# Kernel optimization log

Hardware: AMD Instinct MI355X
Metric: run time of the kernel (lower is better)

Reference implementation:

```python
import jax, jax.numpy as jnp
import numpy as np

B, T, IN = 4096, 64, 3
D, H, NB = 128, 4, 2
DH = D // H  # 32
EPS = 1e-5


def layer_norm(x, g, b):
    mu = x.mean(-1, keepdims=True)
    v = x.var(-1, keepdims=True)
    return (x - mu) / jnp.sqrt(v + EPS) * g + b


def group_norm(x, g, b):
    # headwise GroupNorm over the last dim split into H groups of DH
    xr = x.reshape(x.shape[:-1] + (H, DH))
    mu = xr.mean(-1, keepdims=True)
    v = xr.var(-1, keepdims=True)
    xn = ((xr - mu) / jnp.sqrt(v + EPS)).reshape(x.shape)
    return xn * g + b


def slstm(xg, R):
    # xg: [B,T,4,D] input-driven gate preactivations (i,f,z,o)
    # R : [4,H,DH,DH] block-diagonal (per-head) recurrent kernels per gate
    Bb = xg.shape[0]

    def step(carry, g):
        h, c, n, m = carry  # each [B,D]
        r = jnp.einsum('bhd,ghde->bghe', h.reshape(Bb, H, DH), R).reshape(Bb, 4, D)
        g = g + r
        it, ft, zt, ot = g[:, 0], g[:, 1], g[:, 2], g[:, 3]
        m_new = jnp.maximum(ft + m, it)          # stabilizer state
        i = jnp.exp(it - m_new)                  # stabilized exp input gate
        f = jnp.exp(ft + m - m_new)              # stabilized exp forget gate
        c_new = f * c + i * jnp.tanh(zt)
        n_new = f * n + i                        # normalizer state
        h_new = jax.nn.sigmoid(ot) * c_new / n_new
        return (h_new, c_new, n_new, m_new), h_new

    init = tuple(jnp.zeros((Bb, D), xg.dtype) for _ in range(4))
    _, hs = jax.lax.scan(step, init, jnp.swapaxes(xg, 0, 1))  # [T,B,D]
    return jnp.swapaxes(hs, 0, 1)


def setup_inputs() -> dict:
    key = jax.random.key(0)
    ks = jax.random.split(key, 12)
    s_in = 1.0 / np.sqrt(IN)
    s_d = 1.0 / np.sqrt(D)
    inp = {
        'x': jax.random.normal(ks[0], (B, T, IN), jnp.float32),
        'w_in': jax.random.normal(ks[1], (IN, D), jnp.float32) * s_in,
        'b_in': jnp.zeros((D,), jnp.float32),
        'ln1_g': jnp.ones((NB, D), jnp.float32),
        'ln1_b': jnp.zeros((NB, D), jnp.float32),
        'Wg': jax.random.normal(ks[2], (NB, D, 4 * D), jnp.float32) * s_d,
        'bg': jnp.zeros((NB, 4 * D), jnp.float32),
        'Rg': jax.random.normal(ks[3], (NB, 4, H, DH, DH), jnp.float32) / np.sqrt(DH),
        'gn_g': jnp.ones((NB, D), jnp.float32),
        'gn_b': jnp.zeros((NB, D), jnp.float32),
        'ln2_g': jnp.ones((NB, D), jnp.float32),
        'ln2_b': jnp.zeros((NB, D), jnp.float32),
        'W1': jax.random.normal(ks[4], (NB, D, D), jnp.float32) * s_d,
        'W2': jax.random.normal(ks[5], (NB, D, D), jnp.float32) * s_d,
        'lnf_g': jnp.ones((D,), jnp.float32),
        'lnf_b': jnp.zeros((D,), jnp.float32),
        'w_out': jax.random.normal(ks[6], (D, 1), jnp.float32) * s_d,
        'b_out': jnp.zeros((1,), jnp.float32),
    }
    return inp


def reference(x, w_in, b_in, ln1_g, ln1_b, Wg, bg, Rg, gn_g, gn_b,
              ln2_g, ln2_b, W1, W2, lnf_g, lnf_b, w_out, b_out):
    h = x @ w_in + b_in  # [B,T,D]
    for blk in range(NB):
        # sLSTM sub-block (pre-LN residual)
        xn = layer_norm(h, ln1_g[blk], ln1_b[blk])
        xg = (xn @ Wg[blk] + bg[blk]).reshape(h.shape[0], T, 4, D)
        hs = slstm(xg, Rg[blk])
        h = h + group_norm(hs, gn_g[blk], gn_b[blk])
        # FFN sub-block (pre-LN residual, proj_factor=1.0, gelu, no bias)
        yn = layer_norm(h, ln2_g[blk], ln2_b[blk])
        h = h + jax.nn.gelu(yn @ W1[blk]) @ W2[blk]
    h = layer_norm(h, lnf_g, lnf_b)  # post-blocks norm
    out = (h[:, -1, :] @ w_out + b_out)[:, 0]  # [B]
    return out
```

## Files before the change

kernel.cpp:

```cpp
#include <hip/hip_runtime.h>
#include <hip/hip_bf16.h>
#include <cstdint>
#include <cstddef>

#define EPS 1e-5f
#define BB 4096
#define TT 64
#define NBLK 2
#define MROWS (BB * TT)

typedef unsigned short ushort_t;
typedef __attribute__((ext_vector_type(8))) short short8;
typedef __attribute__((ext_vector_type(4))) float floatx4;

__device__ __forceinline__ ushort_t f2b(float f) {
    __hip_bfloat16 h = __float2bfloat16(f);
    return *reinterpret_cast<ushort_t*>(&h);
}
__device__ __forceinline__ float tanh_fast(float z) {
    return 1.f - 2.f / (__expf(2.f * z) + 1.f);
}
__device__ __forceinline__ float rcp_f(float x) {
    return __builtin_amdgcn_rcpf(x);
}
__device__ __forceinline__ void lds_barrier() {
    asm volatile("s_waitcnt lgkmcnt(0)\n\ts_barrier" ::: "memory");
}

template <int CTRL>
__device__ __forceinline__ float ror_add(float v) {
    int r = __builtin_amdgcn_update_dpp(
        0, __builtin_bit_cast(int, v), CTRL, 0xf, 0xf, false);
    return v + __builtin_bit_cast(float, r);
}
__device__ __forceinline__ float red16(float v) {
    v = ror_add<0x121>(v);
    v = ror_add<0x122>(v);
    v = ror_add<0x124>(v);
    v = ror_add<0x128>(v);
    return v;
}

__global__ __launch_bounds__(256) void k_cvtall(
    const float* __restrict__ Wg, const float* __restrict__ W1,
    const float* __restrict__ W2, ushort_t* __restrict__ Wgt,
    ushort_t* __restrict__ W1t, ushort_t* __restrict__ W2t) {
    int idx = blockIdx.x * 256 + threadIdx.x;
    if (idx < 2 * 512 * 128) {
        int blk = idx >> 16, r = idx & 65535;
        int k = r >> 9, n = r & 511;
        Wgt[(size_t)blk * 65536 + n * 128 + k] = f2b(Wg[idx]);
    } else if (idx < 2 * 512 * 128 + 2 * 128 * 128) {
        int i2 = idx - 2 * 512 * 128;
        int blk = i2 >> 14, r = i2 & 16383;
        int k = r >> 7, n = r & 127;
        W1t[(size_t)blk * 16384 + n * 128 + k] = f2b(W1[i2]);
    } else {
        int i2 = idx - (2 * 512 * 128 + 2 * 128 * 128);
        int blk = i2 >> 14, r = i2 & 16383;
        int k = r >> 7, n = r & 127;
        W2t[(size_t)blk * 16384 + n * 128 + k] = f2b(W2[i2]);
    }
}

template <bool EMBED, bool LASTONLY>
__global__ __launch_bounds__(512, 2) void k_gslstm(
    float* __restrict__ h, const float* __restrict__ x,
    const float* __restrict__ w_in, const float* __restrict__ b_in,
    const ushort_t* __restrict__ Wgt, const float* __restrict__ bg,
    const float* __restrict__ Rg,
    const float* __restrict__ ln1g, const float* __restrict__ ln1b,
    const float* __restrict__ gng, const float* __restrict__ gnb) {
    __shared__ float xg_ring[2][512][16];
    __shared__ ushort_t Afrag[2][16][136];
    __shared__ ushort_t tpose[4][16][40];

    const int tid = threadIdx.x;
    const int lane = tid & 63;
    const int wave = tid >> 6;
    const int q = lane >> 4;
    const int ml = lane & 15;
    const int b0 = blockIdx.x * 16;
    const int xc = ((q + (ml >> 1)) & 3) * 4;

    if (wave < 4) {
        const int p = wave;
        const int row = p * 4 + q;
        short8 WB[4][8];
#pragma unroll
        for (int ks = 0; ks < 4; ++ks)
#pragma unroll
            for (int s = 0; s < 8; ++s)
                WB[ks][s] = *(const short8*)(Wgt +
                    ((size_t)(p * 128 + s * 16 + ml) * 128 + ks * 32 + q * 8));
        float biasv[8];
#pragma unroll
        for (int s = 0; s < 8; ++s) biasv[s] = bg[p * 128 + s * 16 + ml];

        const float4 Lg0 = *(const float4*)(ln1g + ml * 8);
        const float4 Lg1 = *(const float4*)(ln1g + ml * 8 + 4);
        const float4 Lb0 = *(const float4*)(ln1b + ml * 8);
        const float4 Lb1 = *(const float4*)(ln1b + ml * 8 + 4);
        float4 W00{}, W01{}, W10{}, W11{}, W20{}, W21{}, BE0{}, BE1{};
        if (EMBED) {
            W00 = *(const float4*)(w_in + 0 * 128 + ml * 8);
            W01 = *(const float4*)(w_in + 0 * 128 + ml * 8 + 4);
            W10 = *(const float4*)(w_in + 1 * 128 + ml * 8);
            W11 = *(const float4*)(w_in + 1 * 128 + ml * 8 + 4);
            W20 = *(const float4*)(w_in + 2 * 128 + ml * 8);
            W21 = *(const float4*)(w_in + 2 * 128 + ml * 8 + 4);
            BE0 = *(const float4*)(b_in + ml * 8);
            BE1 = *(const float4*)(b_in + ml * 8 + 4);
        }

        auto issue_in = [&](int tt, float4& A, float4& B) {
            const float4* hp =
                (const float4*)(h + ((size_t)(b0 + row) * TT + tt) * 128 + ml * 8);
            A = hp[0]; B = hp[1];
        };
        auto issue_x = [&](int tt, float& x0, float& x1, float& x2) {
            const float* xp = x + ((size_t)(b0 + row) * TT + tt) * 3;
            x0 = xp[0]; x1 = xp[1]; x2 = xp[2];
        };
        auto embed_v = [&](float x0, float x1, float x2, float* v) {
            const float w0[8] = {W00.x, W00.y, W00.z, W00.w, W01.x, W01.y, W01.z, W01.w};
            const float w1[8] = {W10.x, W10.y, W10.z, W10.w, W11.x, W11.y, W11.z, W11.w};
            const float w2[8] = {W20.x, W20.y, W20.z, W20.w, W21.x, W21.y, W21.z, W21.w};
            const float be[8] = {BE0.x, BE0.y, BE0.z, BE0.w, BE1.x, BE1.y, BE1.z, BE1.w};
#pragma unroll
            for (int j = 0; j < 8; ++j)
                v[j] = x0 * w0[j] + x1 * w1[j] + x2 * w2[j] + be[j];
        };
        auto ln_stage = [&](const float* v, int aslot) {
            float s = 0.f, ss = 0.f;
#pragma unroll
            for (int j = 0; j < 8; ++j) { s += v[j]; ss += v[j] * v[j]; }
            s = red16(s);
            ss = red16(ss);
            float mu = s * (1.f / 128.f);
            float rstd = rsqrtf(ss * (1.f / 128.f) - mu * mu + EPS);
            const float gg[8] = {Lg0.x, Lg0.y, Lg0.z, Lg0.w, Lg1.x, Lg1.y, Lg1.z, Lg1.w};
            const float bbv[8] = {Lb0.x, Lb0.y, Lb0.z, Lb0.w, Lb1.x, Lb1.y, Lb1.z, Lb1.w};
            ushort_t pk[8];
#pragma unroll
            for (int j = 0; j < 8; ++j)
                pk[j] = f2b((v[j] - mu) * rstd * gg[j] + bbv[j]);
            *(short8*)&Afrag[aslot][row][ml * 8] = *(const short8*)pk;
        };
        auto gemm_stage = [&](int slot) {
            short8 af[4];
#pragma unroll
            for (int ks = 0; ks < 4; ++ks)
                af[ks] = *(const short8*)&Afrag[slot][ml][ks * 32 + q * 8];
            floatx4 acc[8];
#pragma unroll
            for (int s = 0; s < 8; ++s) {
                float b = biasv[s];
                acc[s] = (floatx4){b, b, b, b};
            }
#pragma unroll
            for (int ks = 0; ks < 4; ++ks)
#pragma unroll
                for (int s = 0; s < 8; ++s)
                    acc[s] = __builtin_amdgcn_mfma_f32_16x16x32_bf16(
                        af[ks], WB[ks][s], acc[s], 0, 0, 0);
#pragma unroll
            for (int s = 0; s < 8; ++s)
                *(floatx4*)&xg_ring[slot][p * 128 + s * 16 + ml][xc] = acc[s];
        };

        float4 pA0, pA1, pB0, pB1;
        float px0 = 0.f, px1 = 0.f, px2 = 0.f, qx0 = 0.f, qx1 = 0.f, qx2 = 0.f;
        {
            float v[8];
            if (EMBED) {
                float a0, a1, a2, d0, d1, d2v;
                issue_x(0, a0, a1, a2);
                issue_x(1, d0, d1, d2v);
                issue_x(2, px0, px1, px2);
                embed_v(a0, a1, a2, v);  ln_stage(v, 0);
                embed_v(d0, d1, d2v, v); ln_stage(v, 1);
            } else {
                float4 a0, a1, d0, d1;
                issue_in(0, a0, a1);
                issue_in(1, d0, d1);
                issue_in(2, pA0, pA1);
                *(float4*)v = a0; *(float4*)(v + 4) = a1; ln_stage(v, 0);
                *(float4*)v = d0; *(float4*)(v + 4) = d1; ln_stage(v, 1);
            }
        }
        lds_barrier();
        gemm_stage(0);
        lds_barrier();

#pragma unroll 1
        for (int t = 0; t < TT; t += 2) {
            if (t + 3 < TT) {
                if (EMBED) issue_x(t + 3, qx0, qx1, qx2);
                else       issue_in(t + 3, pB0, pB1);
            }
            gemm_stage((t + 1) & 1);
            if (t + 2 < TT) {
                float v[8];
                if (EMBED) embed_v(px0, px1, px2, v);
                else { *(float4*)v = pA0; *(float4*)(v + 4) = pA1; }
                ln_stage(v, t & 1);
            }
            lds_barrier();
            if (t + 4 < TT) {
                if (EMBED) issue_x(t + 4, px0, px1, px2);
                else       issue_in(t + 4, pA0, pA1);
            }
            if (t + 2 < TT) gemm_stage(t & 1);
            if (t + 3 < TT) {
                float v[8];
                if (EMBED) embed_v(qx0, qx1, qx2, v);
                else { *(float4*)v = pB0; *(float4*)(v + 4) = pB1; }
                ln_stage(v, (t + 1) & 1);
            }
            lds_barrier();
        }
    } else {
        __builtin_amdgcn_s_setprio(1);
        const int hd = wave - 4;
        short8 RB[4][2];
#pragma unroll
        for (int g = 0; g < 4; ++g)
#pragma unroll
            for (int d2 = 0; d2 < 2; ++d2) {
                ushort_t tmp[8];
#pragma unroll
                for (int j = 0; j < 8; ++j)
                    tmp[j] = f2b(Rg[(size_t)g * 4096 + hd * 1024 +
                                    (q * 8 + j) * 32 + d2 * 16 + ml]);
                RB[g][d2] = *(const short8*)tmp;
            }
        const float gng0 = gng[hd * 32 + ml], gng1 = gng[hd * 32 + 16 + ml];
        const float gnb0 = gnb[hd * 32 + ml], gnb1 = gnb[hd * 32 + 16 + ml];
        float we[3][2], beh[2];
        if (EMBED) {
#pragma unroll
            for (int d2 = 0; d2 < 2; ++d2) {
#pragma unroll
                for (int c = 0; c < 3; ++c)
                    we[c][d2] = w_in[c * 128 + hd * 32 + d2 * 16 + ml];
                beh[d2] = b_in[hd * 32 + d2 * 16 + ml];
            }
        }
        float cst[8], nst[8], mst[8];
#pragma unroll
        for (int i = 0; i < 8; ++i) { cst[i] = 0.f; nst[i] = 0.f; mst[i] = 0.f; }
        {
            ushort_t* tp = &tpose[hd][0][0];
            for (int i = lane; i < 16 * 40; i += 64) tp[i] = 0;
        }

        auto scan_iter = [&](int t) {
            const bool doGN = (!LASTONLY || t == TT - 1);
            float xv[4][3];
            float hg[4][2];
            if (doGN) {
                if (EMBED) {
#pragma unroll
                    for (int r = 0; r < 4; ++r) {
                        const float* xp =
                            x + ((size_t)(b0 + q * 4 + r) * TT + t) * 3;
                        xv[r][0] = xp[0]; xv[r][1] = xp[1]; xv[r][2] = xp[2];
                    }
                } else {
#pragma unroll
                    for (int r = 0; r < 4; ++r)
#pragma unroll
                        for (int d2 = 0; d2 < 2; ++d2)
                            hg[r][d2] = h[((size_t)(b0 + q * 4 + r) * TT + t) * 128 +
                                          hd * 32 + d2 * 16 + ml];
                }
            }
            short8 h8 = *(const short8*)&tpose[hd][ml][q * 8];
            floatx4 acc[4][2];
#pragma unroll
            for (int g = 0; g < 4; ++g)
#pragma unroll
                for (int d2 = 0; d2 < 2; ++d2)
                    acc[g][d2] = *(const floatx4*)
                        &xg_ring[t & 1][g * 128 + hd * 32 + d2 * 16 + ml][xc];
#pragma unroll
            for (int g = 0; g < 4; ++g)
#pragma unroll
                for (int d2 = 0; d2 < 2; ++d2)
                    acc[g][d2] = __builtin_amdgcn_mfma_f32_16x16x32_bf16(
                        h8, RB[g][d2], acc[g][d2], 0, 0, 0);
            float hv[2][4];
#pragma unroll
            for (int d2 = 0; d2 < 2; ++d2)
#pragma unroll
                for (int r = 0; r < 4; ++r) {
                    const int si = d2 * 4 + r;
                    float it = acc[0][d2][r], ft = acc[1][d2][r];
                    float zt = acc[2][d2][r], ot = acc[3][d2][r];
                    float mn = fmaxf(ft + mst[si], it);
                    float iv = __expf(it - mn);
                    float fv = __expf(ft + mst[si] - mn);
                    float e2 = __expf(2.f * zt);
                    float th = 1.f - 2.f * rcp_f(e2 + 1.f);
                    float cn = fv * cst[si] + iv * th;
                    float nn = fv * nst[si] + iv;
                    float eo = __expf(-ot);
                    hv[d2][r] = cn * rcp_f(nn + nn * eo);
                    cst[si] = cn; nst[si] = nn; mst[si] = mn;
                }
#pragma unroll
            for (int d2 = 0; d2 < 2; ++d2)
#pragma unroll
                for (int r = 0; r < 4; ++r)
                    tpose[hd][q * 4 + r][d2 * 16 + ml] = f2b(hv[d2][r]);
            if (doGN) {
                float hinv[4][2];
#pragma unroll
                for (int r = 0; r < 4; ++r)
#pragma unroll
                    for (int d2 = 0; d2 < 2; ++d2) {
                        if (EMBED)
                            hinv[r][d2] = xv[r][0] * we[0][d2] +
                                          xv[r][1] * we[1][d2] +
                                          xv[r][2] * we[2][d2] + beh[d2];
                        else
                            hinv[r][d2] = hg[r][d2];
                    }
                float s[4], ss[4];
#pragma unroll
                for (int r = 0; r < 4; ++r) {
                    s[r] = hv[0][r] + hv[1][r];
                    ss[r] = hv[0][r] * hv[0][r] + hv[1][r] * hv[1][r];
                }
#pragma unroll
                for (int r = 0; r < 4; ++r) {
                    s[r] = red16(s[r]);
                    ss[r] = red16(ss[r]);
                }
#pragma unroll
                for (int r = 0; r < 4; ++r) {
                    float mu = s[r] * (1.f / 32.f);
                    float rstd = rsqrtf(ss[r] * (1.f / 32.f) - mu * mu + EPS);
#pragma unroll
                    for (int d2 = 0; d2 < 2; ++d2) {
                        float gv = d2 ? gng1 : gng0;
                        float bv = d2 ? gnb1 : gnb0;
                        h[((size_t)(b0 + q * 4 + r) * TT + t) * 128 +
                          hd * 32 + d2 * 16 + ml] =
                            hinv[r][d2] + (hv[d2][r] - mu) * rstd * gv + bv;
                    }
                }
            }
        };

        lds_barrier();
        lds_barrier();
#pragma unroll 1
        for (int t = 0; t < TT; t += 2) {
            scan_iter(t);
            lds_barrier();
            scan_iter(t + 1);
            lds_barrier();
        }
    }
}

template <int NT>
__global__ __launch_bounds__(256, 3) void k_ffn_pipe(
    float* __restrict__ h, const ushort_t* __restrict__ W1t,
    const ushort_t* __restrict__ W2t,
    const float* __restrict__ lng, const float* __restrict__ lnb) {
    __shared__ float Hraw[32][132];
    __shared__ ushort_t T1[32][136];
    __shared__ __align__(16) char Ubuf[32 * 132 * 4];
    auto As = (ushort_t(*)[136])Ubuf;
    auto T2 = (float(*)[132])Ubuf;

    int tid = threadIdx.x;
    int lane = tid & 63, wave = tid >> 6;
    int q = lane >> 4, ml = lane & 15;
    int wn = wave * 32;
    int r = tid >> 3, qd = tid & 7;
    int hi = lane >> 5, lo = lane & 31;
    size_t base = (size_t)blockIdx.x * (32 * NT);

    short8 W1B[2][4];
#pragma unroll
    for (int jn = 0; jn < 2; ++jn)
#pragma unroll
        for (int ks = 0; ks < 4; ++ks)
            W1B[jn][ks] = *(const short8*)(W1t +
                ((size_t)(wn + jn * 16 + ml) * 128 + ks * 32 + q * 8));

    float4 cur[4], nxt[4];
#pragma unroll
    for (int k = 0; k < 4; ++k)
        cur[k] = *(const float4*)(h + (base + wave * 8 + 2 * k + hi) * 128 + lo * 4);

#pragma unroll 1
    for (int it = 0; it < NT; ++it) {
#pragma unroll
        for (int k = 0; k < 4; ++k)
            *(float4*)&Hraw[wave * 8 + 2 * k + hi][lo * 4] = cur[k];
        if (it + 1 < NT) {
#pragma unroll
            for (int k = 0; k < 4; ++k)
                nxt[k] = *(const float4*)(h +
                    (base + (it + 1) * 32 + wave * 8 + 2 * k + hi) * 128 + lo * 4);
        }
        lds_barrier();

        float4 hv[4];
#pragma unroll
        for (int k = 0; k < 4; ++k)
            hv[k] = *(const float4*)&Hraw[r][qd * 16 + k * 4];
        float s = 0.f, ss = 0.f;
#pragma unroll
        for (int k = 0; k < 4; ++k) {
            float4 v = hv[k];
            s += v.x + v.y + v.z + v.w;
            ss += v.x * v.x + v.y * v.y + v.z * v.z + v.w * v.w;
        }
        s += __shfl_xor(s, 1); ss += __shfl_xor(ss, 1);
        s += __shfl_xor(s, 2); ss += __shfl_xor(ss, 2);
        s += __shfl_xor(s, 4); ss += __shfl_xor(ss, 4);
        float mu = s * (1.f / 128.f);
        float rstd = rsqrtf(ss * (1.f / 128.f) - mu * mu + EPS);
#pragma unroll
        for (int kk = 0; kk < 2; ++kk) {
            float4 a = hv[2 * kk];
            float4 b = hv[2 * kk + 1];
            int c0 = qd * 16 + kk * 8;
            float4 g0 = *(const float4*)(lng + c0);
            float4 g1 = *(const float4*)(lng + c0 + 4);
            float4 b0 = *(const float4*)(lnb + c0);
            float4 b1 = *(const float4*)(lnb + c0 + 4);
            ushort_t p[8];
            p[0] = f2b((a.x - mu) * rstd * g0.x + b0.x);
            p[1] = f2b((a.y - mu) * rstd * g0.y + b0.y);
            p[2] = f2b((a.z - mu) * rstd * g0.z + b0.z);
            p[3] = f2b((a.w - mu) * rstd * g0.w + b0.w);
            p[4] = f2b((b.x - mu) * rstd * g1.x + b1.x);
            p[5] = f2b((b.y - mu) * rstd * g1.y + b1.y);
            p[6] = f2b((b.z - mu) * rstd * g1.z + b1.z);
            p[7] = f2b((b.w - mu) * rstd * g1.w + b1.w);
            *(short8*)&As[r][c0] = *(const short8*)p;
        }
        lds_barrier();

        floatx4 acc[2][2];
#pragma unroll
        for (int i = 0; i < 2; ++i)
#pragma unroll
            for (int j = 0; j < 2; ++j) acc[i][j] = (floatx4)0.f;
#pragma unroll
        for (int ks = 0; ks < 4; ++ks) {
            short8 af[2];
#pragma unroll
            for (int im = 0; im < 2; ++im)
                af[im] = *(const short8*)&As[im * 16 + ml][ks * 32 + q * 8];
#pragma unroll
            for (int im = 0; im < 2; ++im)
#pragma unroll
                for (int jn = 0; jn < 2; ++jn)
                    acc[im][jn] = __builtin_amdgcn_mfma_f32_16x16x32_bf16(
                        af[im], W1B[jn][ks], acc[im][jn], 0, 0, 0);
        }
#pragma unroll
        for (int im = 0; im < 2; ++im)
#pragma unroll
            for (int jn = 0; jn < 2; ++jn)
#pragma unroll
                for (int rr = 0; rr < 4; ++rr) {
                    float v = acc[im][jn][rr];
                    float u = 0.7978845608028654f * (v + 0.044715f * v * v * v);
                    float gv = 0.5f * v * (1.f + tanh_fast(u));
                    T1[im * 16 + q * 4 + rr][wn + jn * 16 + ml] = f2b(gv);
                }
        short8 W2B[2][4];
#pragma unroll
        for (int jn = 0; jn < 2; ++jn)
#pragma unroll
            for (int ks = 0; ks < 4; ++ks)
                W2B[jn][ks] = *(const short8*)(W2t +
                    ((size_t)(wn + jn * 16 + ml) * 128 + ks * 32 + q * 8));
        lds_barrier();

#pragma unroll
        for (int i = 0; i < 2; ++i)
#pragma unroll
            for (int j = 0; j < 2; ++j) acc[i][j] = (floatx4)0.f;
#pragma unroll
        for (int ks = 0; ks < 4; ++ks) {
            short8 af[2];
#pragma unroll
            for (int im = 0; im < 2; ++im)
                af[im] = *(const short8*)&T1[im * 16 + ml][ks * 32 + q * 8];
#pragma unroll
            for (int im = 0; im < 2; ++im)
#pragma unroll
                for (int jn = 0; jn < 2; ++jn)
                    acc[im][jn] = __builtin_amdgcn_mfma_f32_16x16x32_bf16(
                        af[im], W2B[jn][ks], acc[im][jn], 0, 0, 0);
        }
#pragma unroll
        for (int im = 0; im < 2; ++im)
#pragma unroll
            for (int jn = 0; jn < 2; ++jn)
#pragma unroll
                for (int rr = 0; rr < 4; ++rr)
                    T2[im * 16 + q * 4 + rr][wn + jn * 16 + ml] = acc[im][jn][rr];
        lds_barrier();

#pragma unroll
        for (int k = 0; k < 4; ++k) {
            float4 t2v = *(const float4*)&T2[wave * 8 + 2 * k + hi][lo * 4];
            float4 o;
            o.x = cur[k].x + t2v.x;
            o.y = cur[k].y + t2v.y;
            o.z = cur[k].z + t2v.z;
            o.w = cur[k].w + t2v.w;
            *(float4*)(h + (base + it * 32 + wave * 8 + 2 * k + hi) * 128 + lo * 4) = o;
        }
        if (it + 1 < NT) {
#pragma unroll
            for (int k = 0; k < 4; ++k) cur[k] = nxt[k];
        }
    }
}

__global__ __launch_bounds__(256, 6) void k_tail(
    const float* __restrict__ h, const ushort_t* __restrict__ W1t,
    const ushort_t* __restrict__ W2t,
    const float* __restrict__ lng, const float* __restrict__ lnb,
    const float* __restrict__ lnfg, const float* __restrict__ lnfb,
    const float* __restrict__ w_out, const float* __restrict__ b_out,
    float* __restrict__ out) {
    __shared__ __align__(16) char U[32 * 136 * 2 * 2];
    auto As = (ushort_t(*)[136])U;
    auto T1 = (ushort_t(*)[136])(U + 32 * 136 * 2);
    auto F = (float(*)[136])U;
    int tid = threadIdx.x;
    int lane = tid & 63, wave = tid >> 6;
    int q = lane >> 4, ml = lane & 15;
    int wn = wave * 32;
    size_t row0 = (size_t)blockIdx.x * 32;

    short8 W1B[2][4];
#pragma unroll
    for (int jn = 0; jn < 2; ++jn)
#pragma unroll
        for (int ks = 0; ks < 4; ++ks)
            W1B[jn][ks] = *(const short8*)(W1t +
                ((size_t)(wn + jn * 16 + ml) * 128 + ks * 32 + q * 8));

    int r = tid >> 3, qd = tid & 7;
    size_t grow = (row0 + r) * TT + (TT - 1);
    const float* hrow = h + grow * 128 + qd * 16;
    float s = 0.f, ss = 0.f;
#pragma unroll
    for (int k = 0; k < 4; ++k) {
        float4 v = ((const float4*)hrow)[k];
        s += v.x + v.y + v.z + v.w;
        ss += v.x * v.x + v.y * v.y + v.z * v.z + v.w * v.w;
    }
    s += __shfl_xor(s, 1); ss += __shfl_xor(ss, 1);
    s += __shfl_xor(s, 2); ss += __shfl_xor(ss, 2);
    s += __shfl_xor(s, 4); ss += __shfl_xor(ss, 4);
    float mu = s * (1.f / 128.f);
    float rstd = rsqrtf(ss * (1.f / 128.f) - mu * mu + EPS);
#pragma unroll
    for (int kk = 0; kk < 2; ++kk) {
        float4 a = ((const float4*)hrow)[2 * kk];
        float4 b = ((const float4*)hrow)[2 * kk + 1];
        int c0 = qd * 16 + kk * 8;
        float4 g0 = *(const float4*)(lng + c0);
        float4 g1 = *(const float4*)(lng + c0 + 4);
        float4 b0 = *(const float4*)(lnb + c0);
        float4 b1 = *(const float4*)(lnb + c0 + 4);
        ushort_t p[8];
        p[0] = f2b((a.x - mu) * rstd * g0.x + b0.x);
        p[1] = f2b((a.y - mu) * rstd * g0.y + b0.y);
        p[2] = f2b((a.z - mu) * rstd * g0.z + b0.z);
        p[3] = f2b((a.w - mu) * rstd * g0.w + b0.w);
        p[4] = f2b((b.x - mu) * rstd * g1.x + b1.x);
        p[5] = f2b((b.y - mu) * rstd * g1.y + b1.y);
        p[6] = f2b((b.z - mu) * rstd * g1.z + b1.z);
        p[7] = f2b((b.w - mu) * rstd * g1.w + b1.w);
        *(short8*)&As[r][c0] = *(const short8*)p;
    }
    lds_barrier();

    floatx4 acc[2][2];
#pragma unroll
    for (int i = 0; i < 2; ++i)
#pragma unroll
        for (int j = 0; j < 2; ++j) acc[i][j] = (floatx4)0.f;
#pragma unroll
    for (int ks = 0; ks < 4; ++ks) {
        short8 af[2];
#pragma unroll
        for (int im = 0; im < 2; ++im)
            af[im] = *(const short8*)&As[im * 16 + ml][ks * 32 + q * 8];
#pragma unroll
        for (int im = 0; im < 2; ++im)
#pragma unroll
            for (int jn = 0; jn < 2; ++jn)
                acc[im][jn] = __builtin_amdgcn_mfma_f32_16x16x32_bf16(
                    af[im], W1B[jn][ks], acc[im][jn], 0, 0, 0);
    }
#pragma unroll
    for (int im = 0; im < 2; ++im)
#pragma unroll
        for (int jn = 0; jn < 2; ++jn)
#pragma unroll
            for (int rr = 0; rr < 4; ++rr) {
                float v = acc[im][jn][rr];
                float u = 0.7978845608028654f * (v + 0.044715f * v * v * v);
                float gv = 0.5f * v * (1.f + tanh_fast(u));
                T1[im * 16 + q * 4 + rr][wn + jn * 16 + ml] = f2b(gv);
            }
    short8 W2B[2][4];
#pragma unroll
    for (int jn = 0; jn < 2; ++jn)
#pragma unroll
        for (int ks = 0; ks < 4; ++ks)
            W2B[jn][ks] = *(const short8*)(W2t +
                ((size_t)(wn + jn * 16 + ml) * 128 + ks * 32 + q * 8));
    lds_barrier();

    float rres[2][2][4];
#pragma unroll
    for (int im = 0; im < 2; ++im)
#pragma unroll
        for (int jn = 0; jn < 2; ++jn)
#pragma unroll
            for (int rr = 0; rr < 4; ++rr) {
                int rloc = im * 16 + q * 4 + rr;
                rres[im][jn][rr] = h[((row0 + rloc) * TT + (TT - 1)) * 128 +
                                     wn + jn * 16 + ml];
            }
#pragma unroll
    for (int i = 0; i < 2; ++i)
#pragma unroll
        for (int j = 0; j < 2; ++j) acc[i][j] = (floatx4)0.f;
#pragma unroll
    for (int ks = 0; ks < 4; ++ks) {
        short8 af[2];
#pragma unroll
        for (int im = 0; im < 2; ++im)
            af[im] = *(const short8*)&T1[im * 16 + ml][ks * 32 + q * 8];
#pragma unroll
        for (int im = 0; im < 2; ++im)
#pragma unroll
            for (int jn = 0; jn < 2; ++jn)
                acc[im][jn] = __builtin_amdgcn_mfma_f32_16x16x32_bf16(
                    af[im], W2B[jn][ks], acc[im][jn], 0, 0, 0);
    }
    lds_barrier();
#pragma unroll
    for (int im = 0; im < 2; ++im)
#pragma unroll
        for (int jn = 0; jn < 2; ++jn)
#pragma unroll
            for (int rr = 0; rr < 4; ++rr) {
                int rloc = im * 16 + q * 4 + rr;
                F[rloc][wn + jn * 16 + ml] = rres[im][jn][rr] + acc[im][jn][rr];
            }
    lds_barrier();

    float4 fv[4];
#pragma unroll
    for (int k = 0; k < 4; ++k)
        fv[k] = *(const float4*)&F[r][qd * 16 + k * 4];
    float s2 = 0.f, ss2 = 0.f;
#pragma unroll
    for (int k = 0; k < 4; ++k) {
        float4 v = fv[k];
        s2 += v.x + v.y + v.z + v.w;
        ss2 += v.x * v.x + v.y * v.y + v.z * v.z + v.w * v.w;
    }
    s2 += __shfl_xor(s2, 1); ss2 += __shfl_xor(ss2, 1);
    s2 += __shfl_xor(s2, 2); ss2 += __shfl_xor(ss2, 2);
    s2 += __shfl_xor(s2, 4); ss2 += __shfl_xor(ss2, 4);
    float mu2 = s2 * (1.f / 128.f);
    float rstd2 = rsqrtf(ss2 * (1.f / 128.f) - mu2 * mu2 + EPS);
    float dot = 0.f;
#pragma unroll
    for (int k = 0; k < 4; ++k) {
        int c0 = qd * 16 + k * 4;
        float4 g = *(const float4*)(lnfg + c0);
        float4 bb = *(const float4*)(lnfb + c0);
        float4 w = *(const float4*)(w_out + c0);
        dot += ((fv[k].x - mu2) * rstd2 * g.x + bb.x) * w.x +
               ((fv[k].y - mu2) * rstd2 * g.y + bb.y) * w.y +
               ((fv[k].z - mu2) * rstd2 * g.z + bb.z) * w.z +
               ((fv[k].w - mu2) * rstd2 * g.w + bb.w) * w.w;
    }
    dot += __shfl_xor(dot, 1);
    dot += __shfl_xor(dot, 2);
    dot += __shfl_xor(dot, 4);
    if (qd == 0) out[row0 + r] = dot + b_out[0];
}

extern "C" void kernel_launch(void* const* d_in, const int* in_sizes, int n_in,
                              void* d_out, int out_size, void* d_ws, size_t ws_size,
                              hipStream_t stream) {
    const float* x    = (const float*)d_in[0];
    const float* w_in = (const float*)d_in[1];
    const float* b_in = (const float*)d_in[2];
    const float* ln1g = (const float*)d_in[3];
    const float* ln1b = (const float*)d_in[4];
    const float* Wg   = (const float*)d_in[5];
    const float* bg   = (const float*)d_in[6];
    const float* Rg   = (const float*)d_in[7];
    const float* gng  = (const float*)d_in[8];
    const float* gnb  = (const float*)d_in[9];
    const float* ln2g = (const float*)d_in[10];
    const float* ln2b = (const float*)d_in[11];
    const float* W1   = (const float*)d_in[12];
    const float* W2   = (const float*)d_in[13];
    const float* lnfg = (const float*)d_in[14];
    const float* lnfb = (const float*)d_in[15];
    const float* wout = (const float*)d_in[16];
    const float* bout = (const float*)d_in[17];
    float* out = (float*)d_out;

    float* h = (float*)d_ws;
    ushort_t* Wgt = (ushort_t*)(h + (size_t)MROWS * 128);
    ushort_t* W1t = Wgt + 2 * 512 * 128;
    ushort_t* W2t = W1t + 2 * 128 * 128;

    k_cvtall<<<(2 * 512 * 128 + 4 * 128 * 128) / 256, 256, 0, stream>>>(
        Wg, W1, W2, Wgt, W1t, W2t);

    k_gslstm<true, false><<<BB / 16, 512, 0, stream>>>(
        h, x, w_in, b_in, Wgt, bg, Rg, ln1g, ln1b, gng, gnb);
    k_ffn_pipe<8><<<MROWS / 256, 256, 0, stream>>>(h, W1t, W2t, ln2g, ln2b);
    k_gslstm<false, true><<<BB / 16, 512, 0, stream>>>(
        h, nullptr, nullptr, nullptr, Wgt + (size_t)512 * 128, bg + 512,
        Rg + (size_t)16384, ln1g + 128, ln1b + 128, gng + 128, gnb + 128);
    k_tail<<<BB / 32, 256, 0, stream>>>(h, W1t + 16384, W2t + 16384,
                                        ln2g + 128, ln2b + 128,
                                        lnfg, lnfb, wout, bout, out);
}
```

Measured before the change: 330.0 us.

## Replace block-pipelined FFN kernel with barrier-free per-wave 16-row FFN

Rewrites the middle FFN kernel so that each wave independently handles 16 rows. It loads those rows straight into registers as MFMA A-fragments, computes LayerNorm with cross-lane shuffles, and runs both GEMMs using only private per-wave LDS scratch, so it needs no block barriers. This removes the block-wide s_barrier synchronisation and the staging of h through shared LDS. In exchange, every wave reloads all of W1 and W2 from global/L2, where before each block kept them in registers across 8 tiles. The grid also grows to many small blocks without the prefetch pipeline.

```diff
diff --git a/kernel.cpp b/kernel.cpp
--- a/kernel.cpp
+++ b/kernel.cpp
@@ -25,6 +25,9 @@
 }
 __device__ __forceinline__ void lds_barrier() {
     asm volatile("s_waitcnt lgkmcnt(0)\n\ts_barrier" ::: "memory");
+}
+__device__ __forceinline__ void ds_wait() {
+    asm volatile("s_waitcnt lgkmcnt(0)" ::: "memory");
 }
 
 template <int CTRL>
@@ -366,167 +369,110 @@
     }
 }
 
-template <int NT>
-__global__ __launch_bounds__(256, 3) void k_ffn_pipe(
+__global__ __launch_bounds__(256) void k_ffn_wave(
     float* __restrict__ h, const ushort_t* __restrict__ W1t,
     const ushort_t* __restrict__ W2t,
     const float* __restrict__ lng, const float* __restrict__ lnb) {
-    __shared__ float Hraw[32][132];
-    __shared__ ushort_t T1[32][136];
-    __shared__ __align__(16) char Ubuf[32 * 132 * 4];
-    auto As = (ushort_t(*)[136])Ubuf;
-    auto T2 = (float(*)[132])Ubuf;
-
-    int tid = threadIdx.x;
-    int lane = tid & 63, wave = tid >> 6;
-    int q = lane >> 4, ml = lane & 15;
-    int wn = wave * 32;
-    int r = tid >> 3, qd = tid & 7;
-    int hi = lane >> 5, lo = lane & 31;
-    size_t base = (size_t)blockIdx.x * (32 * NT);
-
-    short8 W1B[2][4];
-#pragma unroll
-    for (int jn = 0; jn < 2; ++jn)
+    __shared__ __align__(16) char LDSU[4][16 * 132 * 4];
+    const int tid = threadIdx.x;
+    const int lane = tid & 63, wave = tid >> 6;
+    const int q = lane >> 4, ml = lane & 15;
+    auto tp = (ushort_t(*)[136])(LDSU[wave]);
+    auto ot = (float(*)[132])(LDSU[wave]);
+    const size_t row0 = (size_t)(blockIdx.x * 4 + wave) * 16;
+
+    float* hp = h + (row0 + ml) * 128;
+    float4 raw[8];
+#pragma unroll
+    for (int ks = 0; ks < 4; ++ks) {
+        raw[2 * ks]     = *(const float4*)(hp + ks * 32 + q * 8);
+        raw[2 * ks + 1] = *(const float4*)(hp + ks * 32 + q * 8 + 4);
+    }
+    float s = 0.f, ss = 0.f;
+#pragma unroll
+    for (int i = 0; i < 8; ++i) {
+        float4 v = raw[i];
+        s += v.x + v.y + v.z + v.w;
+        ss += v.x * v.x + v.y * v.y + v.z * v.z + v.w * v.w;
+    }
+    s += __shfl_xor(s, 16); ss += __shfl_xor(ss, 16);
+    s += __shfl_xor(s, 32); ss += __shfl_xor(ss, 32);
+    float mu = s * (1.f / 128.f);
+    float rstd = rsqrtf(ss * (1.f / 128.f) - mu * mu + EPS);
+
+    short8 af[4];
+#pragma unroll
+    for (int ks = 0; ks < 4; ++ks) {
+        int c0 = ks * 32 + q * 8;
+        float4 g0 = *(const float4*)(lng + c0);
+        float4 g1 = *(const float4*)(lng + c0 + 4);
+        float4 b0 = *(const float4*)(lnb + c0);
+        float4 b1 = *(const float4*)(lnb + c0 + 4);
+        float4 a = raw[2 * ks], b = raw[2 * ks + 1];
+        ushort_t p[8];
+        p[0] = f2b((a.x - mu) * rstd * g0.x + b0.x);
+        p[1] = f2b((a.y - mu) * rstd * g0.y + b0.y);
+        p[2] = f2b((a.z - mu) * rstd * g0.z + b0.z);
+        p[3] = f2b((a.w - mu) * rstd * g0.w + b0.w);
+        p[4] = f2b((b.x - mu) * rstd * g1.x + b1.x);
+        p[5] = f2b((b.y - mu) * rstd * g1.y + b1.y);
+        p[6] = f2b((b.z - mu) * rstd * g1.z + b1.z);
+        p[7] = f2b((b.w - mu) * rstd * g1.w + b1.w);
+        af[ks] = *(const short8*)p;
+    }
+
+#pragma unroll
+    for (int cn = 0; cn < 8; ++cn) {
+        short8 WB[4];
 #pragma unroll
         for (int ks = 0; ks < 4; ++ks)
-            W1B[jn][ks] = *(const short8*)(W1t +
-                ((size_t)(wn + jn * 16 + ml) * 128 + ks * 32 + q * 8));
-
-    float4 cur[4], nxt[4];
-#pragma unroll
-    for (int k = 0; k < 4; ++k)
-        cur[k] = *(const float4*)(h + (base + wave * 8 + 2 * k + hi) * 128 + lo * 4);
-
-#pragma unroll 1
-    for (int it = 0; it < NT; ++it) {
-#pragma unroll
-        for (int k = 0; k < 4; ++k)
-            *(float4*)&Hraw[wave * 8 + 2 * k + hi][lo * 4] = cur[k];
-        if (it + 1 < NT) {
-#pragma unroll
-            for (int k = 0; k < 4; ++k)
-                nxt[k] = *(const float4*)(h +
-                    (base + (it + 1) * 32 + wave * 8 + 2 * k + hi) * 128 + lo * 4);
+            WB[ks] = *(const short8*)(W1t +
+                ((size_t)(cn * 16 + ml) * 128 + ks * 32 + q * 8));
+        floatx4 acc = (floatx4)0.f;
+#pragma unroll
+        for (int ks = 0; ks < 4; ++ks)
+            acc = __builtin_amdgcn_mfma_f32_16x16x32_bf16(af[ks], WB[ks], acc, 0, 0, 0);
+#pragma unroll
+        for (int rr = 0; rr < 4; ++rr) {
+            float v = acc[rr];
+            float u = 0.7978845608028654f * (v + 0.044715f * v * v * v);
+            float gv = 0.5f * v * (1.f + tanh_fast(u));
+            tp[q * 4 + rr][cn * 16 + ml] = f2b(gv);
         }
-        lds_barrier();
-
-        float4 hv[4];
-#pragma unroll
-        for (int k = 0; k < 4; ++k)
-            hv[k] = *(const float4*)&Hraw[r][qd * 16 + k * 4];
-        float s = 0.f, ss = 0.f;
-#pragma unroll
-        for (int k = 0; k < 4; ++k) {
-            float4 v = hv[k];
-            s += v.x + v.y + v.z + v.w;
-            ss += v.x * v.x + v.y * v.y + v.z * v.z + v.w * v.w;
-        }
-        s += __shfl_xor(s, 1); ss += __shfl_xor(ss, 1);
-        s += __shfl_xor(s, 2); ss += __shfl_xor(ss, 2);
-        s += __shfl_xor(s, 4); ss += __shfl_xor(ss, 4);
-        float mu = s * (1.f / 128.f);
-        float rstd = rsqrtf(ss * (1.f / 128.f) - mu * mu + EPS);
-#pragma unroll
-        for (int kk = 0; kk < 2; ++kk) {
-            float4 a = hv[2 * kk];
-            float4 b = hv[2 * kk + 1];
-            int c0 = qd * 16 + kk * 8;
-            float4 g0 = *(const float4*)(lng + c0);
-            float4 g1 = *(const float4*)(lng + c0 + 4);
-            float4 b0 = *(const float4*)(lnb + c0);
-            float4 b1 = *(const float4*)(lnb + c0 + 4);
-            ushort_t p[8];
-            p[0] = f2b((a.x - mu) * rstd * g0.x + b0.x);
-            p[1] = f2b((a.y - mu) * rstd * g0.y + b0.y);
-            p[2] = f2b((a.z - mu) * rstd * g0.z + b0.z);
-            p[3] = f2b((a.w - mu) * rstd * g0.w + b0.w);
-            p[4] = f2b((b.x - mu) * rstd * g1.x + b1.x);
-            p[5] = f2b((b.y - mu) * rstd * g1.y + b1.y);
-            p[6] = f2b((b.z - mu) * rstd * g1.z + b1.z);
-            p[7] = f2b((b.w - mu) * rstd * g1.w + b1.w);
-            *(short8*)&As[r][c0] = *(const short8*)p;
-        }
-        lds_barrier();
-
-        floatx4 acc[2][2];
-#pragma unroll
-        for (int i = 0; i < 2; ++i)
-#pragma unroll
-            for (int j = 0; j < 2; ++j) acc[i][j] = (floatx4)0.f;
-#pragma unroll
-        for (int ks = 0; ks < 4; ++ks) {
-            short8 af[2];
-#pragma unroll
-            for (int im = 0; im < 2; ++im)
-                af[im] = *(const short8*)&As[im * 16 + ml][ks * 32 + q * 8];
-#pragma unroll
-            for (int im = 0; im < 2; ++im)
-#pragma unroll
-                for (int jn = 0; jn < 2; ++jn)
-                    acc[im][jn] = __builtin_amdgcn_mfma_f32_16x16x32_bf16(
-                        af[im], W1B[jn][ks], acc[im][jn], 0, 0, 0);
-        }
-#pragma unroll
-        for (int im = 0; im < 2; ++im)
-#pragma unroll
-            for (int jn = 0; jn < 2; ++jn)
-#pragma unroll
-                for (int rr = 0; rr < 4; ++rr) {
-                    float v = acc[im][jn][rr];
-                    float u = 0.7978845608028654f * (v + 0.044715f * v * v * v);
-                    float gv = 0.5f * v * (1.f + tanh_fast(u));
-                    T1[im * 16 + q * 4 + rr][wn + jn * 16 + ml] = f2b(gv);
-                }
-        short8 W2B[2][4];
-#pragma unroll
-        for (int jn = 0; jn < 2; ++jn)
-#pragma unroll
-            for (int ks = 0; ks < 4; ++ks)
-                W2B[jn][ks] = *(const short8*)(W2t +
-                    ((size_t)(wn + jn * 16 + ml) * 128 + ks * 32 + q * 8));
-        lds_barrier();
-
-#pragma unroll
-        for (int i = 0; i < 2; ++i)
-#pragma unroll
-            for (int j = 0; j < 2; ++j) acc[i][j] = (floatx4)0.f;
-#pragma unroll
-        for (int ks = 0; ks < 4; ++ks) {
-            short8 af[2];
-#pragma unroll
-            for (int im = 0; im < 2; ++im)
-                af[im] = *(const short8*)&T1[im * 16 + ml][ks * 32 + q * 8];
-#pragma unroll
-            for (int im = 0; im < 2; ++im)
-#pragma unroll
-                for (int jn = 0; jn < 2; ++jn)
-                    acc[im][jn] = __builtin_amdgcn_mfma_f32_16x16x32_bf16(
-                        af[im], W2B[jn][ks], acc[im][jn], 0, 0, 0);
-        }
-#pragma unroll
-        for (int im = 0; im < 2; ++im)
-#pragma unroll
-            for (int jn = 0; jn < 2; ++jn)
-#pragma unroll
-                for (int rr = 0; rr < 4; ++rr)
-                    T2[im * 16 + q * 4 + rr][wn + jn * 16 + ml] = acc[im][jn][rr];
-        lds_barrier();
-
-#pragma unroll
-        for (int k = 0; k < 4; ++k) {
-            float4 t2v = *(const float4*)&T2[wave * 8 + 2 * k + hi][lo * 4];
-            float4 o;
-            o.x = cur[k].x + t2v.x;
-            o.y = cur[k].y + t2v.y;
-            o.z = cur[k].z + t2v.z;
-            o.w = cur[k].w + t2v.w;
-            *(float4*)(h + (base + it * 32 + wave * 8 + 2 * k + hi) * 128 + lo * 4) = o;
-        }
-        if (it + 1 < NT) {
-#pragma unroll
-            for (int k = 0; k < 4; ++k) cur[k] = nxt[k];
-        }
+    }
+    ds_wait();
+
+    short8 a2[4];
+#pragma unroll
+    for (int ks = 0; ks < 4; ++ks)
+        a2[ks] = *(const short8*)&tp[ml][ks * 32 + q * 8];
+
+#pragma unroll
+    for (int cn = 0; cn < 8; ++cn) {
+        short8 WB[4];
+#pragma unroll
+        for (int ks = 0; ks < 4; ++ks)
+            WB[ks] = *(const short8*)(W2t +
+                ((size_t)(cn * 16 + ml) * 128 + ks * 32 + q * 8));
+        floatx4 acc = (floatx4)0.f;
+#pragma unroll
+        for (int ks = 0; ks < 4; ++ks)
+            acc = __builtin_amdgcn_mfma_f32_16x16x32_bf16(a2[ks], WB[ks], acc, 0, 0, 0);
+#pragma unroll
+        for (int rr = 0; rr < 4; ++rr)
+            ot[q * 4 + rr][cn * 16 + ml] = acc[rr];
+    }
+    ds_wait();
+
+#pragma unroll
+    for (int ks = 0; ks < 4; ++ks) {
+        float4 o0 = *(const float4*)&ot[ml][ks * 32 + q * 8];
+        float4 o1 = *(const float4*)&ot[ml][ks * 32 + q * 8 + 4];
+        float4 a = raw[2 * ks], b = raw[2 * ks + 1];
+        o0.x += a.x; o0.y += a.y; o0.z += a.z; o0.w += a.w;
+        o1.x += b.x; o1.y += b.y; o1.z += b.z; o1.w += b.w;
+        *(float4*)(hp + ks * 32 + q * 8) = o0;
+        *(float4*)(hp + ks * 32 + q * 8 + 4) = o1;
     }
 }
 
@@ -737,7 +683,7 @@
 
     k_gslstm<true, false><<<BB / 16, 512, 0, stream>>>(
         h, x, w_in, b_in, Wgt, bg, Rg, ln1g, ln1b, gng, gnb);
-    k_ffn_pipe<8><<<MROWS / 256, 256, 0, stream>>>(h, W1t, W2t, ln2g, ln2b);
+    k_ffn_wave<<<MROWS / 64, 256, 0, stream>>>(h, W1t, W2t, ln2g, ln2b);
     k_gslstm<false, true><<<BB / 16, 512, 0, stream>>>(
         h, nullptr, nullptr, nullptr, Wgt + (size_t)512 * 128, bg + 512,
         Rg + (size_t)16384, ln1g + 128, ln1b + 128, gng + 128, gnb + 128);
```

Measured after the change: 392.1 us. 18.8% more time.
